# Kernel tuning notes

Hardware: AMD Instinct MI355X
Metric: run time of the kernel (lower is better)

The kernel has to match this reference:

```python
import jax, jax.numpy as jnp
import numpy as np

B, G, K, N, M, E, L = 8, 512, 64, 1024, 128, 4, 5

def _lin(x, w, b):
    return x @ w.T + b

def setup_inputs():
    key = jax.random.key(0)
    ks = jax.random.split(key, 20)
    def nrm(k, shape, s=1.0):
        return jax.random.normal(k, shape, dtype=jnp.float32) * s
    def lin_p(k, out_d, in_d):
        k1, k2 = jax.random.split(k)
        s = 1.0 / float(np.sqrt(in_d))
        return nrm(k1, (out_d, in_d), s), nrm(k2, (out_d,), s)
    inp = {}
    inp["z"] = nrm(ks[0], (B, G, K, M), 0.5)
    inp["hs_grid"] = nrm(ks[1], (B, G, M))
    inp["hs_key"] = nrm(ks[2], (B, K, M))
    inp["lig_rep"] = nrm(ks[3], (B, E))
    inp["hs_rec"] = nrm(ks[4], (B, N, M))
    inp["w_Rl"] = jnp.ones((1,), dtype=jnp.float32)
    inp["w_mask"] = jax.random.randint(ks[5], (B, K), 0, 2)
    dims = {"wra": (M, M), "wrh": (M, M), "wla": (M, M), "wlh": (M, M),
            "z1": (1, M), "wcR": (M, M), "wcl": (M, M), "kR": (M, M),
            "mapL": (L, 2 * M + E), "fin": (1, L)}
    for i, nm in enumerate(dims):
        w, b = lin_p(ks[6 + i], *dims[nm])
        inp[nm + "_w"] = w
        inp[nm + "_b"] = b
    return inp

def reference(z, hs_grid, hs_key, lig_rep, hs_rec, w_Rl, w_mask,
              wra_w, wra_b, wrh_w, wrh_b, wla_w, wla_b, wlh_w, wlh_b,
              z1_w, z1_b, wcR_w, wcR_b, wcl_w, wcl_b, kR_w, kR_b,
              mapL_w, mapL_b, fin_w, fin_b):
    exp_z = jnp.exp(z)                                    # [B,G,K,M]
    zr = exp_z / exp_z.sum(axis=-2, keepdims=True)        # pseudo-softmax over K
    ra = jnp.einsum('bgkm,bkm->bgm', zr, hs_key)          # [B,G,M]
    zl = exp_z / exp_z.sum(axis=-3, keepdims=True)        # pseudo-softmax over G
    la = jnp.einsum('bgkm,bgm->bkm', zl, hs_grid)         # [B,K,M]
    ra_rh = _lin(ra, wra_w, wra_b) + _lin(hs_grid, wrh_w, wrh_b)  # [B,G,M]
    la_lh = _lin(la, wla_w, wla_b) + _lin(hs_key, wlh_w, wlh_b)   # [B,K,M]
    att = _lin(z, z1_w, z1_b)[..., 0]                     # [B,G,K]
    att_l = jax.nn.softmax(att, axis=2).sum(axis=1)       # [B,K]
    att_r = jax.nn.softmax(att, axis=1).sum(axis=2)       # [B,G]
    key_rep = jnp.einsum('bk,bkm->bm', att_l, la_lh)      # [B,M]
    grid_rep = jnp.einsum('bg,bgm->bm', att_r, ra_rh)     # [B,M]
    Rh = _lin(hs_rec, wcR_w, wcR_b)                       # [B,N,M]
    lh = _lin(hs_key, wcl_w, wcl_b)                       # [B,K,M]
    z_Rl = jnp.einsum('bnh,bkh->bnk', Rh, lh)             # [B,N,K]
    masked = jnp.where(w_mask[:, None, :] == 0, jnp.float32(-1e10), w_Rl * z_Rl)
    z_Rl = jax.nn.softmax(masked, axis=1)                 # softmax over N
    kfr = jnp.einsum('bnk,bnh->bkh', z_Rl, hs_rec)        # [B,K,M]
    kfr = _lin(kfr, kR_w, kR_b)
    kfr = jnp.einsum('bk,bkh->bh', att_l, kfr)            # [B,M]
    key_rep = key_rep + kfr
    pair_rep = jnp.concatenate([key_rep, lig_rep, grid_rep], axis=1)  # [B,2M+E]
    pair_rep = _lin(pair_rep, mapL_w, mapL_b)             # [B,L]
    return _lin(pair_rep, fin_w, fin_b)[..., 0]           # [B]
```

## Files before the change

kernel.cpp:

```cpp
#include <hip/hip_runtime.h>

#define Bb 8
#define Gg 512
#define Kk 64
#define Nn 1024
#define Mm 128
#define KM (Kk * Mm)
#define GPB 16
#define NCH 32

struct P7 { const float* p[7]; };

__global__ __launch_bounds__(1024) void kA(
    const float* __restrict__ z, const float* __restrict__ hs_grid,
    const float* __restrict__ hs_key, const float* __restrict__ z1w,
    P7 ptrs, float* __restrict__ wT,
    float* __restrict__ raOut, float* __restrict__ attOut,
    float* __restrict__ laNum, float* __restrict__ laDen)
{
  __shared__ __align__(16) float smem[10240];
  const int bid = blockIdx.x;
  const int t = threadIdx.x;

  if (bid >= Bb * NCH) {
    float* tile = smem;
    const int r = bid - Bb * NCH;
    const int mat = r >> 4, tl = r & 15;
    const int xo = (tl & 3) * 32, y0 = (tl >> 2) * 32;
    const int tx = t & 31, ty = t >> 5;
    const float* src = ptrs.p[mat];
    float* dst = wT + (size_t)mat * Mm * Mm;
    tile[ty * 33 + tx] = src[(size_t)(y0 + ty) * Mm + xo + tx];
    __syncthreads();
    dst[(size_t)(xo + ty) * Mm + y0 + tx] = tile[tx * 33 + ty];
    return;
  }

  float* s_hsgrid = smem;
  float* s_rn     = smem + 2048;
  float* s_rd     = smem + 6144;

  const int b = bid >> 5;
  const int gblk = bid & 31;
  const int lane_m = t & 31;
  const int m4 = lane_m << 2;
  const int kgrp = t >> 5;
  const int wv = t >> 6;

  const float* hgb = hs_grid + ((size_t)b * Gg + gblk * GPB) * Mm;
  for (int idx = t; idx < GPB * Mm; idx += 1024) s_hsgrid[idx] = hgb[idx];

  const int ofs0 = (kgrp * 2) * Mm + m4;
  const int ofs1 = ofs0 + Mm;
  const float4 hk0 = *reinterpret_cast<const float4*>(hs_key + (size_t)b * KM + ofs0);
  const float4 hk1 = *reinterpret_cast<const float4*>(hs_key + (size_t)b * KM + ofs1);

  const float zw0 = z1w[m4], zw1 = z1w[m4 + 1], zw2 = z1w[m4 + 2], zw3 = z1w[m4 + 3];

  float la_n[2][4], la_d[2][4];
#pragma unroll
  for (int i = 0; i < 2; ++i)
#pragma unroll
    for (int j = 0; j < 4; ++j) { la_n[i][j] = 0.f; la_d[i][j] = 0.f; }

  const float* zb = z + ((size_t)b * Gg + gblk * GPB) * (size_t)KM;
  float4 c0 = *reinterpret_cast<const float4*>(zb + ofs0);
  float4 c1 = *reinterpret_cast<const float4*>(zb + ofs1);

  __syncthreads();

  for (int gl = 0; gl < GPB; ++gl) {
    float4 n0 = c0, n1 = c1;
    if (gl < GPB - 1) {
      n0 = *reinterpret_cast<const float4*>(zb + (size_t)(gl + 1) * KM + ofs0);
      n1 = *reinterpret_cast<const float4*>(zb + (size_t)(gl + 1) * KM + ofs1);
    }
    const int g = gblk * GPB + gl;
    const float4 hg = *reinterpret_cast<const float4*>(s_hsgrid + gl * Mm + m4);
    float rn0 = 0, rn1 = 0, rn2 = 0, rn3 = 0, rd0 = 0, rd1 = 0, rd2 = 0, rd3 = 0;
#pragma unroll
    for (int i = 0; i < 2; ++i) {
      const float4 v = (i == 0) ? c0 : c1;
      const float4 hk = (i == 0) ? hk0 : hk1;
      const int k = kgrp * 2 + i;
      const float e0 = __expf(v.x), e1 = __expf(v.y), e2 = __expf(v.z), e3 = __expf(v.w);
      la_n[i][0] += e0 * hg.x; la_n[i][1] += e1 * hg.y; la_n[i][2] += e2 * hg.z; la_n[i][3] += e3 * hg.w;
      la_d[i][0] += e0;        la_d[i][1] += e1;        la_d[i][2] += e2;        la_d[i][3] += e3;
      rn0 += e0 * hk.x; rn1 += e1 * hk.y; rn2 += e2 * hk.z; rn3 += e3 * hk.w;
      rd0 += e0; rd1 += e1; rd2 += e2; rd3 += e3;
      float ap = v.x * zw0 + v.y * zw1 + v.z * zw2 + v.w * zw3;
      ap += __shfl_xor(ap, 16); ap += __shfl_xor(ap, 8); ap += __shfl_xor(ap, 4);
      ap += __shfl_xor(ap, 2);  ap += __shfl_xor(ap, 1);
      if (lane_m == 0) attOut[((size_t)b * Gg + g) * Kk + k] = ap;
    }
    rn0 += __shfl_xor(rn0, 32); rn1 += __shfl_xor(rn1, 32); rn2 += __shfl_xor(rn2, 32); rn3 += __shfl_xor(rn3, 32);
    rd0 += __shfl_xor(rd0, 32); rd1 += __shfl_xor(rd1, 32); rd2 += __shfl_xor(rd2, 32); rd3 += __shfl_xor(rd3, 32);
    float* rnB = s_rn + (gl & 1) * 2048;
    float* rdB = s_rd + (gl & 1) * 2048;
    if ((t & 63) < 32) {
      *reinterpret_cast<float4*>(rnB + wv * Mm + m4) = make_float4(rn0, rn1, rn2, rn3);
      *reinterpret_cast<float4*>(rdB + wv * Mm + m4) = make_float4(rd0, rd1, rd2, rd3);
    }
    __syncthreads();
    if (t < Mm) {
      float num = 0.f, den = 0.f;
#pragma unroll
      for (int ww = 0; ww < 16; ++ww) { num += rnB[ww * Mm + t]; den += rdB[ww * Mm + t]; }
      raOut[((size_t)b * Gg + g) * Mm + t] = num / den;
    }
    c0 = n0; c1 = n1;
  }

  const size_t base = ((size_t)(b * NCH + gblk)) * KM;
#pragma unroll
  for (int i = 0; i < 2; ++i) {
    const int k = kgrp * 2 + i;
    *reinterpret_cast<float4*>(laNum + base + k * Mm + m4) =
        make_float4(la_n[i][0], la_n[i][1], la_n[i][2], la_n[i][3]);
    *reinterpret_cast<float4*>(laDen + base + k * Mm + m4) =
        make_float4(la_d[i][0], la_d[i][1], la_d[i][2], la_d[i][3]);
  }
}

__global__ __launch_bounds__(256) void kB(
    const float* __restrict__ laNum, const float* __restrict__ laDen, float* __restrict__ la,
    const float* __restrict__ att, float* __restrict__ attlP,
    float* __restrict__ attrPM, float* __restrict__ attrPS,
    const float* __restrict__ hs_key, const float* __restrict__ wT,
    const float* __restrict__ wcR_w, const float* __restrict__ wcl_b,
    float* __restrict__ Lk)
{
  __shared__ __align__(16) float smem[1088];
  const int bid = blockIdx.x;
  const int t = threadIdx.x;

  if (bid < 256) {
    const int idx = bid * 256 + t;
    const int b = idx >> 13, r = idx & 8191;
    const float* np = laNum + (size_t)b * NCH * KM + r;
    const float* dp = laDen + (size_t)b * NCH * KM + r;
    float num = 0.f, den = 0.f;
#pragma unroll 8
    for (int p = 0; p < NCH; ++p) { num += np[(size_t)p * KM]; den += dp[(size_t)p * KM]; }
    la[idx] = num / den;
  } else if (bid < 320) {
    const int blk = bid - 256;
    const int b = blk >> 3, p = blk & 7;
    const int w = t >> 6, lane = t & 63;
    float acc = 0.f;
    for (int j = 0; j < 16; ++j) {
      const int g = p * 64 + w * 16 + j;
      const float a = att[((size_t)b * Gg + g) * Kk + lane];
      float mx = a;
      for (int off = 32; off; off >>= 1) mx = fmaxf(mx, __shfl_xor(mx, off));
      const float e = __expf(a - mx);
      float s = e;
      for (int off = 32; off; off >>= 1) s += __shfl_xor(s, off);
      acc += e / s;
    }
    float* sred = smem;
    sred[w * 64 + lane] = acc;
    __syncthreads();
    if (t < 64) attlP[(b * 8 + p) * 64 + t] = sred[t] + sred[64 + t] + sred[128 + t] + sred[192 + t];
  } else if (bid < 384) {
    const int blk = bid - 320;
    const int b = blk >> 3, gc = blk & 7;
    const int k = t & 63, j4 = t >> 6;
    float m = -1e30f, s = 0.f;
    for (int j = 0; j < 16; ++j) {
      const int g = gc * 64 + j4 * 16 + j;
      const float a = att[((size_t)b * Gg + g) * Kk + k];
      if (a > m) { s = s * __expf(m - a) + 1.0f; m = a; }
      else s += __expf(a - m);
    }
    float* sm = smem;
    float* ss = smem + 256;
    sm[j4 * 64 + k] = m; ss[j4 * 64 + k] = s;
    __syncthreads();
    if (t < 64) {
      float M = sm[t];
      for (int q = 1; q < 4; ++q) M = fmaxf(M, sm[q * 64 + t]);
      float S = 0.f;
      for (int q = 0; q < 4; ++q) S += ss[q * 64 + t] * __expf(sm[q * 64 + t] - M);
      attrPM[(b * 8 + gc) * 64 + t] = M;
      attrPS[(b * 8 + gc) * 64 + t] = S;
    }
  } else {
    const int blk = bid - 384;
    const int b = blk >> 3, k8 = blk & 7;
    float* s_lh = smem;
    const int m = t & 127;
    const int half = __builtin_amdgcn_readfirstlane(t >> 7);
    const float* wclT = wT + 5 * 16384;
    {
      const float* keyb = hs_key + ((size_t)b * Kk + k8 * 8 + half * 4) * Mm;
      float a0 = 0.f, a1 = 0.f, a2 = 0.f, a3 = 0.f;
      for (int h4 = 0; h4 < 32; ++h4) {
        const float4 r0v = *reinterpret_cast<const float4*>(keyb + h4 * 4);
        const float4 r1v = *reinterpret_cast<const float4*>(keyb + 128 + h4 * 4);
        const float4 r2v = *reinterpret_cast<const float4*>(keyb + 256 + h4 * 4);
        const float4 r3v = *reinterpret_cast<const float4*>(keyb + 384 + h4 * 4);
        const float w0 = wclT[(size_t)(h4 * 4 + 0) * Mm + m];
        const float w1 = wclT[(size_t)(h4 * 4 + 1) * Mm + m];
        const float w2 = wclT[(size_t)(h4 * 4 + 2) * Mm + m];
        const float w3 = wclT[(size_t)(h4 * 4 + 3) * Mm + m];
        a0 += r0v.x * w0 + r0v.y * w1 + r0v.z * w2 + r0v.w * w3;
        a1 += r1v.x * w0 + r1v.y * w1 + r1v.z * w2 + r1v.w * w3;
        a2 += r2v.x * w0 + r2v.y * w1 + r2v.z * w2 + r2v.w * w3;
        a3 += r3v.x * w0 + r3v.y * w1 + r3v.z * w2 + r3v.w * w3;
      }
      const float bm = wcl_b[m];
      s_lh[(half * 4 + 0) * 132 + m] = a0 + bm;
      s_lh[(half * 4 + 1) * 132 + m] = a1 + bm;
      s_lh[(half * 4 + 2) * 132 + m] = a2 + bm;
      s_lh[(half * 4 + 3) * 132 + m] = a3 + bm;
    }
    __syncthreads();
    {
      const int h = m;
      const int r0 = half * 4;
      float b0 = 0.f, b1 = 0.f, b2 = 0.f, b3 = 0.f;
      for (int mq = 0; mq < 32; ++mq) {
        const float4 L0 = *reinterpret_cast<const float4*>(&s_lh[(r0 + 0) * 132 + mq * 4]);
        const float4 L1 = *reinterpret_cast<const float4*>(&s_lh[(r0 + 1) * 132 + mq * 4]);
        const float4 L2 = *reinterpret_cast<const float4*>(&s_lh[(r0 + 2) * 132 + mq * 4]);
        const float4 L3 = *reinterpret_cast<const float4*>(&s_lh[(r0 + 3) * 132 + mq * 4]);
        const float w0 = wcR_w[(size_t)(mq * 4 + 0) * Mm + h];
        const float w1 = wcR_w[(size_t)(mq * 4 + 1) * Mm + h];
        const float w2 = wcR_w[(size_t)(mq * 4 + 2) * Mm + h];
        const float w3 = wcR_w[(size_t)(mq * 4 + 3) * Mm + h];
        b0 += L0.x * w0 + L0.y * w1 + L0.z * w2 + L0.w * w3;
        b1 += L1.x * w0 + L1.y * w1 + L1.z * w2 + L1.w * w3;
        b2 += L2.x * w0 + L2.y * w1 + L2.z * w2 + L2.w * w3;
        b3 += L3.x * w0 + L3.y * w1 + L3.z * w2 + L3.w * w3;
      }
      const size_t ob = ((size_t)b * Kk + k8 * 8 + r0) * Mm + h;
      Lk[ob] = b0; Lk[ob + Mm] = b1; Lk[ob + 2 * Mm] = b2; Lk[ob + 3 * Mm] = b3;
    }
  }
}

__global__ __launch_bounds__(256) void kC(
    const float* __restrict__ att, const float* __restrict__ attrPM, const float* __restrict__ attrPS,
    float* __restrict__ att_r,
    const float* __restrict__ hs_rec, const float* __restrict__ Lk,
    const int* __restrict__ mask, const float* __restrict__ wRl,
    float* __restrict__ scores, float* __restrict__ pmT, float* __restrict__ psT)
{
  __shared__ __align__(16) float smem[4608];
  const int bid = blockIdx.x;
  const int t = threadIdx.x;

  if (bid < 64) {
    const int b = bid >> 3, gc = bid & 7;
    const int k = t & 63, grp = t >> 6;
    float* Mx = smem;
    float* S = smem + 64;
    if (t < 64) {
      float M = -1e30f;
      for (int p = 0; p < 8; ++p) M = fmaxf(M, attrPM[(b * 8 + p) * 64 + t]);
      float s = 0.f;
      for (int p = 0; p < 8; ++p) s += attrPS[(b * 8 + p) * 64 + t] * __expf(attrPM[(b * 8 + p) * 64 + t] - M);
      Mx[t] = M; S[t] = s;
    }
    __syncthreads();
    const float Mk = Mx[k], Sk = S[k];
    for (int j = 0; j < 16; ++j) {
      const int g = gc * 64 + grp * 16 + j;
      float p = __expf(att[((size_t)b * Gg + g) * Kk + k] - Mk) / Sk;
      for (int off = 32; off; off >>= 1) p += __shfl_xor(p, off);
      if (k == 0) att_r[b * Gg + g] = p;
    }
  } else {
    const int vb = bid - 64;
    const int b = vb >> 6, ntile = vb & 63;
    const int n0 = ntile * 16;
    const int k = t & 63;
    const int hq = __builtin_amdgcn_readfirstlane(t >> 6);
    float rLk[32];
    {
      const float* Lp = Lk + ((size_t)b * Kk + k) * Mm + hq * 32;
#pragma unroll
      for (int j = 0; j < 8; ++j) {
        const float4 v = *reinterpret_cast<const float4*>(Lp + j * 4);
        rLk[j * 4 + 0] = v.x; rLk[j * 4 + 1] = v.y;
        rLk[j * 4 + 2] = v.z; rLk[j * 4 + 3] = v.w;
      }
    }
    float acc[16];
    const float* rb = hs_rec + ((size_t)b * Nn + n0) * Mm + hq * 32;
#pragma unroll
    for (int r = 0; r < 16; ++r) {
      const float* rp = rb + r * Mm;
      float s = 0.f;
#pragma unroll
      for (int j4 = 0; j4 < 8; ++j4) {
        const float4 rv = *reinterpret_cast<const float4*>(rp + j4 * 4);
        s += rv.x * rLk[j4 * 4] + rv.y * rLk[j4 * 4 + 1] +
             rv.z * rLk[j4 * 4 + 2] + rv.w * rLk[j4 * 4 + 3];
      }
      acc[r] = s;
    }
    float* s_acc = smem;
    float* s_m   = smem + 4096;
    float* s_s   = smem + 4352;
#pragma unroll
    for (int r = 0; r < 16; ++r) s_acc[(hq * 16 + r) * 64 + k] = acc[r];
    __syncthreads();
    const float wv = wRl[0];
    const bool msk = (mask[b * Kk + k] == 0);
    float m = -3.0e38f, ssum = 0.f;
    for (int q = 0; q < 4; ++q) {
      const int idx = q * 256 + t;
      const int r = idx >> 6, kk = idx & 63;
      float v = s_acc[r * 64 + kk] + s_acc[(16 + r) * 64 + kk] +
                s_acc[(32 + r) * 64 + kk] + s_acc[(48 + r) * 64 + kk];
      v = msk ? -1e10f : wv * v;
      scores[((size_t)b * Nn + n0 + r) * Kk + kk] = v;
      if (v > m) { ssum = ssum * __expf(m - v) + 1.0f; m = v; }
      else ssum += __expf(v - m);
    }
    s_m[hq * 64 + k] = m; s_s[hq * 64 + k] = ssum;
    __syncthreads();
    if (t < 64) {
      float M = fmaxf(fmaxf(s_m[t], s_m[64 + t]), fmaxf(s_m[128 + t], s_m[192 + t]));
      float S = 0.f;
#pragma unroll
      for (int q = 0; q < 4; ++q) S += s_s[q * 64 + t] * __expf(s_m[q * 64 + t] - M);
      pmT[((size_t)b * 64 + ntile) * 64 + t] = M;
      psT[((size_t)b * 64 + ntile) * 64 + t] = S;
    }
  }
}

__global__ __launch_bounds__(512) void kD(
    const float* __restrict__ scores, const float* __restrict__ hs_rec,
    const float* __restrict__ pmT, const float* __restrict__ psT,
    const float* __restrict__ attlP, const float* __restrict__ att_r,
    const float* __restrict__ ra, const float* __restrict__ hs_grid,
    const float* __restrict__ la, const float* __restrict__ hs_key,
    float* __restrict__ uP, float* __restrict__ w1P, float* __restrict__ w2P,
    float* __restrict__ w0P, float* __restrict__ v1, float* __restrict__ v2,
    float* __restrict__ sAv)
{
  __shared__ float sm[1280];
  __shared__ float s_attl[64];
  __shared__ float sM[64], sSi[64];
  const int bid = blockIdx.x;
  const int t = threadIdx.x;

  if (bid < 64) {
    const int b = bid >> 3, nc = bid & 7;
    if (t < 64) {
      float a = 0.f;
      for (int p = 0; p < 8; ++p) a += attlP[(b * 8 + p) * 64 + t];
      s_attl[t] = a;
      float M = -3.0e38f;
      for (int nt = 0; nt < 64; ++nt) M = fmaxf(M, pmT[((size_t)b * 64 + nt) * 64 + t]);
      float S = 0.f;
      for (int nt = 0; nt < 64; ++nt)
        S += psT[((size_t)b * 64 + nt) * 64 + t] * __expf(pmT[((size_t)b * 64 + nt) * 64 + t] - M);
      sM[t] = M; sSi[t] = 1.0f / S;
    }
    __syncthreads();
    const int n = t >> 2, ks = t & 3;
    const float* sc = scores + ((size_t)b * Nn + nc * 128 + n) * Kk + ks * 16;
    float qp = 0.f;
#pragma unroll
    for (int j = 0; j < 16; ++j) {
      const int k = ks * 16 + j;
      qp += s_attl[k] * __expf(sc[j] - sM[k]) * sSi[k];
    }
    sm[n * 4 + ks] = qp;
    __syncthreads();
    float* q = sm + 512;
    if (t < 128) q[t] = sm[t * 4] + sm[t * 4 + 1] + sm[t * 4 + 2] + sm[t * 4 + 3];
    __syncthreads();
    const int h = t & 127, nq = t >> 7;
    float acc = 0.f;
    const float* hr = hs_rec + ((size_t)b * Nn + nc * 128 + nq * 32) * Mm + h;
    for (int j = 0; j < 32; ++j) acc += q[nq * 32 + j] * hr[(size_t)j * Mm];
    float* red = sm + 640;
    red[nq * 128 + h] = acc;
    __syncthreads();
    if (t < 128) uP[((size_t)b * 8 + nc) * 128 + t] = red[t] + red[128 + t] + red[256 + t] + red[384 + t];
  } else if (bid < 128) {
    const int blk = bid - 64;
    const int b = blk >> 3, gc = blk & 7;
    float* s_ar = sm + 1152;
    if (t < 64) s_ar[t] = att_r[b * Gg + gc * 64 + t];
    __syncthreads();
    const int h = t & 127, gq = t >> 7;
    float a1 = 0.f, a2 = 0.f;
    const float* rp = ra + ((size_t)b * Gg + gc * 64 + gq * 16) * Mm + h;
    const float* gp = hs_grid + ((size_t)b * Gg + gc * 64 + gq * 16) * Mm + h;
    for (int j = 0; j < 16; ++j) {
      const float w = s_ar[gq * 16 + j];
      a1 += w * rp[(size_t)j * Mm];
      a2 += w * gp[(size_t)j * Mm];
    }
    float* r1 = sm;
    float* r2 = sm + 512;
    r1[gq * 128 + h] = a1; r2[gq * 128 + h] = a2;
    __syncthreads();
    if (t < 128) {
      w1P[((size_t)b * 8 + gc) * 128 + t] = r1[t] + r1[128 + t] + r1[256 + t] + r1[384 + t];
      w2P[((size_t)b * 8 + gc) * 128 + t] = r2[t] + r2[128 + t] + r2[256 + t] + r2[384 + t];
    }
    if (t == 0) {
      float s = 0.f;
      for (int j = 0; j < 64; ++j) s += s_ar[j];
      w0P[b * 8 + gc] = s;
    }
  } else {
    const int b = bid - 128;
    if (t < 64) {
      float a = 0.f;
      for (int p = 0; p < 8; ++p) a += attlP[(b * 8 + p) * 64 + t];
      s_attl[t] = a;
    }
    __syncthreads();
    const int h = t & 127, kq = t >> 7;
    float a1 = 0.f, a2 = 0.f;
    const float* lp = la + ((size_t)b * Kk + kq * 16) * Mm + h;
    const float* kp = hs_key + ((size_t)b * Kk + kq * 16) * Mm + h;
    for (int j = 0; j < 16; ++j) {
      const float w = s_attl[kq * 16 + j];
      a1 += w * lp[(size_t)j * Mm];
      a2 += w * kp[(size_t)j * Mm];
    }
    float* r1 = sm;
    float* r2 = sm + 512;
    r1[kq * 128 + h] = a1; r2[kq * 128 + h] = a2;
    __syncthreads();
    if (t < 128) {
      v1[b * 128 + t] = r1[t] + r1[128 + t] + r1[256 + t] + r1[384 + t];
      v2[b * 128 + t] = r2[t] + r2[128 + t] + r2[256 + t] + r2[384 + t];
    }
    if (t == 0) {
      float s = 0.f;
      for (int j = 0; j < 64; ++j) s += s_attl[j];
      sAv[b] = s;
    }
  }
}

__global__ __launch_bounds__(1024) void kE(
    const float* __restrict__ uP, const float* __restrict__ w1P, const float* __restrict__ w2P,
    const float* __restrict__ w0P, const float* __restrict__ v1, const float* __restrict__ v2,
    const float* __restrict__ sAv, const float* __restrict__ wT,
    const float* __restrict__ wra_b, const float* __restrict__ wrh_b,
    const float* __restrict__ wla_b, const float* __restrict__ wlh_b,
    const float* __restrict__ kR_b, const float* __restrict__ lig_rep,
    const float* __restrict__ mapL_w, const float* __restrict__ mapL_b,
    const float* __restrict__ fin_w, const float* __restrict__ fin_b,
    float* __restrict__ out)
{
  __shared__ float sV1[128], sV2[128], sU[128], sW1[128], sW2[128];
  __shared__ float sPair[264];
  __shared__ float sRed[2][8][128];
  __shared__ float s5[8];
  __shared__ float sSc[2];
  const int b = blockIdx.x, t = threadIdx.x;
  const int m = t & 127, hf = t >> 7;

  if (t < 128) {
    float u = 0.f, w1 = 0.f, w2 = 0.f;
    for (int c = 0; c < 8; ++c) {
      u  += uP[((size_t)b * 8 + c) * 128 + t];
      w1 += w1P[((size_t)b * 8 + c) * 128 + t];
      w2 += w2P[((size_t)b * 8 + c) * 128 + t];
    }
    sU[t] = u; sW1[t] = w1; sW2[t] = w2;
    sV1[t] = v1[b * 128 + t]; sV2[t] = v2[b * 128 + t];
  }
  if (t == 0) {
    float s = 0.f;
    for (int c = 0; c < 8; ++c) s += w0P[b * 8 + c];
    sSc[0] = s;
    sSc[1] = sAv[b];
  }
  __syncthreads();

  const float* wraT = wT;
  const float* wrhT = wT + 1 * 16384;
  const float* wlaT = wT + 2 * 16384;
  const float* wlhT = wT + 3 * 16384;
  const float* kRT  = wT + 6 * 16384;
  float key = 0.f, grd = 0.f;
  for (int h = hf * 16; h < hf * 16 + 16; ++h) {
    key += sV1[h] * wlaT[h * Mm + m] + sV2[h] * wlhT[h * Mm + m] + sU[h] * kRT[h * Mm + m];
    grd += sW1[h] * wraT[h * Mm + m] + sW2[h] * wrhT[h * Mm + m];
  }
  sRed[0][hf][m] = key; sRed[1][hf][m] = grd;
  __syncthreads();
  if (t < 128) {
    const float sR = sSc[0], sA = sSc[1];
    float kk = 0.f, gg = 0.f;
#pragma unroll
    for (int q = 0; q < 8; ++q) { kk += sRed[0][q][t]; gg += sRed[1][q][t]; }
    sPair[t] = kk + sA * (wla_b[t] + wlh_b[t] + kR_b[t]);
    sPair[132 + t] = gg + sR * (wra_b[t] + wrh_b[t]);
  }
  if (t < 4) sPair[128 + t] = lig_rep[b * 4 + t];
  __syncthreads();

  const int wq = t >> 6, lane = t & 63;
  if (wq < 5) {
    float acc = 0.f;
    for (int c = lane; c < 260; c += 64) acc += sPair[c] * mapL_w[wq * 260 + c];
    for (int off = 32; off; off >>= 1) acc += __shfl_xor(acc, off);
    if (lane == 0) s5[wq] = acc + mapL_b[wq];
  }
  __syncthreads();
  if (t == 0) {
    float o = fin_b[0];
    for (int l = 0; l < 5; ++l) o += s5[l] * fin_w[l];
    out[b] = o;
  }
}

extern "C" void kernel_launch(void* const* d_in, const int* in_sizes, int n_in,
                              void* d_out, int out_size, void* d_ws, size_t ws_size,
                              hipStream_t stream) {
  const float* z       = (const float*)d_in[0];
  const float* hs_grid = (const float*)d_in[1];
  const float* hs_key  = (const float*)d_in[2];
  const float* lig_rep = (const float*)d_in[3];
  const float* hs_rec  = (const float*)d_in[4];
  const float* w_Rl    = (const float*)d_in[5];
  const int*   w_mask  = (const int*)d_in[6];
  const float* wra_w = (const float*)d_in[7];  const float* wra_b = (const float*)d_in[8];
  const float* wrh_w = (const float*)d_in[9];  const float* wrh_b = (const float*)d_in[10];
  const float* wla_w = (const float*)d_in[11]; const float* wla_b = (const float*)d_in[12];
  const float* wlh_w = (const float*)d_in[13]; const float* wlh_b = (const float*)d_in[14];
  const float* z1_w  = (const float*)d_in[15];
  const float* wcR_w = (const float*)d_in[17]; const float* wcR_b = (const float*)d_in[18];
  const float* wcl_w = (const float*)d_in[19]; const float* wcl_b = (const float*)d_in[20];
  const float* kR_w  = (const float*)d_in[21]; const float* kR_b  = (const float*)d_in[22];
  const float* mapL_w = (const float*)d_in[23]; const float* mapL_b = (const float*)d_in[24];
  const float* fin_w  = (const float*)d_in[25]; const float* fin_b  = (const float*)d_in[26];
  float* out = (float*)d_out;

  float* w = (float*)d_ws;
  float* wT    = w;
  float* ra    = wT + 7 * 16384;
  float* att   = ra + Bb * Gg * Mm;
  float* laNum = att + Bb * Gg * Kk;
  float* laDen = laNum + Bb * NCH * Kk * Mm;
  float* la    = laDen + Bb * NCH * Kk * Mm;
  float* attlP = la + Bb * Kk * Mm;
  float* attrPM = attlP + Bb * 8 * 64;
  float* attrPS = attrPM + Bb * 8 * 64;
  float* att_r = attrPS + Bb * 8 * 64;
  float* Lk    = att_r + Bb * Gg;
  float* scores = Lk + Bb * Kk * Mm;

  float* pmT  = laNum;
  float* psT  = laNum + 32768;
  float* uP   = laNum + 65536;
  float* w1P  = laNum + 73728;
  float* w2P  = laNum + 81920;
  float* w0P  = laNum + 90112;
  float* v1   = laNum + 90176;
  float* v2   = laNum + 91200;
  float* sAv  = laNum + 92224;

  P7 ptrs;
  ptrs.p[0] = wra_w; ptrs.p[1] = wrh_w; ptrs.p[2] = wla_w; ptrs.p[3] = wlh_w;
  ptrs.p[4] = wcR_w; ptrs.p[5] = wcl_w; ptrs.p[6] = kR_w;

  kA<<<Bb * NCH + 112, 1024, 0, stream>>>(z, hs_grid, hs_key, z1_w, ptrs, wT,
                                          ra, att, laNum, laDen);
  kB<<<448, 256, 0, stream>>>(laNum, laDen, la, att, attlP, attrPM, attrPS,
                              hs_key, wT, wcR_w, wcl_b, Lk);
  kC<<<576, 256, 0, stream>>>(att, attrPM, attrPS, att_r, hs_rec, Lk,
                              w_mask, w_Rl, scores, pmT, psT);
  kD<<<136, 512, 0, stream>>>(scores, hs_rec, pmT, psT, attlP, att_r,
                              ra, hs_grid, la, hs_key,
                              uP, w1P, w2P, w0P, v1, v2, sAv);
  kE<<<Bb, 1024, 0, stream>>>(uP, w1P, w2P, w0P, v1, v2, sAv, wT,
                              wra_b, wrh_b, wla_b, wlh_b, kR_b, lig_rep,
                              mapL_w, mapL_b, fin_w, fin_b, out);
}
```

Measured before the change: 89.06 us.

## Fold final linear layers into projected weight vectors and merge pipeline into three kernels

```diff
diff --git a/kernel.cpp b/kernel.cpp
--- a/kernel.cpp
+++ b/kernel.cpp
@@ -9,151 +9,239 @@
 #define GPB 16
 #define NCH 32
 
-struct P7 { const float* p[7]; };
-
-__global__ __launch_bounds__(1024) void kA(
-    const float* __restrict__ z, const float* __restrict__ hs_grid,
-    const float* __restrict__ hs_key, const float* __restrict__ z1w,
-    P7 ptrs, float* __restrict__ wT,
-    float* __restrict__ raOut, float* __restrict__ attOut,
-    float* __restrict__ laNum, float* __restrict__ laDen)
-{
-  __shared__ __align__(16) float smem[10240];
+struct K1Args {
+  const float *z, *hs_grid, *hs_key, *z1w;
+  const float *wra_w, *wrh_w, *wla_w, *wlh_w, *kR_w;
+  const float *wla_b, *wlh_b, *kR_b, *wra_b, *wrh_b;
+  const float *wcl_w, *wcl_b, *wcR_w;
+  const float *mapL_w, *mapL_b, *fin_w, *fin_b;
+  float *att, *laNum, *laDen, *rdot, *Lk, *gbuf;
+};
+
+__global__ __launch_bounds__(1024) void K1(K1Args a) {
+  __shared__ __align__(16) float smem[10496];
   const int bid = blockIdx.x;
   const int t = threadIdx.x;
 
-  if (bid >= Bb * NCH) {
-    float* tile = smem;
-    const int r = bid - Bb * NCH;
-    const int mat = r >> 4, tl = r & 15;
-    const int xo = (tl & 3) * 32, y0 = (tl >> 2) * 32;
-    const int tx = t & 31, ty = t >> 5;
-    const float* src = ptrs.p[mat];
-    float* dst = wT + (size_t)mat * Mm * Mm;
-    tile[ty * 33 + tx] = src[(size_t)(y0 + ty) * Mm + xo + tx];
-    __syncthreads();
-    dst[(size_t)(xo + ty) * Mm + y0 + tx] = tile[tx * 33 + ty];
-    return;
-  }
-
-  float* s_hsgrid = smem;
-  float* s_rn     = smem + 2048;
-  float* s_rd     = smem + 6144;
-
-  const int b = bid >> 5;
-  const int gblk = bid & 31;
-  const int lane_m = t & 31;
-  const int m4 = lane_m << 2;
-  const int kgrp = t >> 5;
-  const int wv = t >> 6;
-
-  const float* hgb = hs_grid + ((size_t)b * Gg + gblk * GPB) * Mm;
-  for (int idx = t; idx < GPB * Mm; idx += 1024) s_hsgrid[idx] = hgb[idx];
-
-  const int ofs0 = (kgrp * 2) * Mm + m4;
-  const int ofs1 = ofs0 + Mm;
-  const float4 hk0 = *reinterpret_cast<const float4*>(hs_key + (size_t)b * KM + ofs0);
-  const float4 hk1 = *reinterpret_cast<const float4*>(hs_key + (size_t)b * KM + ofs1);
-
-  const float zw0 = z1w[m4], zw1 = z1w[m4 + 1], zw2 = z1w[m4 + 2], zw3 = z1w[m4 + 3];
-
-  float la_n[2][4], la_d[2][4];
-#pragma unroll
-  for (int i = 0; i < 2; ++i)
-#pragma unroll
-    for (int j = 0; j < 4; ++j) { la_n[i][j] = 0.f; la_d[i][j] = 0.f; }
-
-  const float* zb = z + ((size_t)b * Gg + gblk * GPB) * (size_t)KM;
-  float4 c0 = *reinterpret_cast<const float4*>(zb + ofs0);
-  float4 c1 = *reinterpret_cast<const float4*>(zb + ofs1);
-
-  __syncthreads();
-
-  for (int gl = 0; gl < GPB; ++gl) {
-    float4 n0 = c0, n1 = c1;
-    if (gl < GPB - 1) {
-      n0 = *reinterpret_cast<const float4*>(zb + (size_t)(gl + 1) * KM + ofs0);
-      n1 = *reinterpret_cast<const float4*>(zb + (size_t)(gl + 1) * KM + ofs1);
-    }
-    const int g = gblk * GPB + gl;
-    const float4 hg = *reinterpret_cast<const float4*>(s_hsgrid + gl * Mm + m4);
-    float rn0 = 0, rn1 = 0, rn2 = 0, rn3 = 0, rd0 = 0, rd1 = 0, rd2 = 0, rd3 = 0;
+  if (bid < 256) {
+    float* s_gw     = smem;
+    float* s_hsgrid = smem + 256;
+    float* s_rn     = smem + 2304;
+    float* s_rd     = smem + 6400;
+    float* s_fvecG  = smem + 2304;
+
+    const int b = bid >> 5;
+    const int gblk = bid & 31;
+    const int lane_m = t & 31;
+    const int m4 = lane_m << 2;
+    const int kgrp = t >> 5;
+    const int wv = t >> 6;
+
+    const int ofs0 = (kgrp * 2) * Mm + m4;
+    const int ofs1 = ofs0 + Mm;
+    const float* zb = a.z + ((size_t)b * Gg + gblk * GPB) * (size_t)KM;
+    float4 c0 = *reinterpret_cast<const float4*>(zb + ofs0);
+    float4 c1 = *reinterpret_cast<const float4*>(zb + ofs1);
+
+    const float* hgb = a.hs_grid + ((size_t)b * Gg + gblk * GPB) * Mm;
+    for (int idx = t; idx < GPB * Mm; idx += 1024) s_hsgrid[idx] = hgb[idx];
+
+    const float4 hk0 = *reinterpret_cast<const float4*>(a.hs_key + (size_t)b * KM + ofs0);
+    const float4 hk1 = *reinterpret_cast<const float4*>(a.hs_key + (size_t)b * KM + ofs1);
+    const float zw0 = a.z1w[m4], zw1 = a.z1w[m4 + 1], zw2 = a.z1w[m4 + 2], zw3 = a.z1w[m4 + 3];
+
+    if (t < 128) {
+      float f = 0.f;
+#pragma unroll
+      for (int l = 0; l < 5; ++l) f += a.fin_w[l] * a.mapL_w[l * 260 + 132 + t];
+      s_fvecG[t] = f;
+    }
+    __syncthreads();
+    if (t < 256) {
+      const int h = t & 127;
+      const float* W = (t >> 7) ? a.wrh_w : a.wra_w;
+      float g = 0.f;
+      for (int mm = 0; mm < 128; ++mm) g += s_fvecG[mm] * W[(size_t)mm * Mm + h];
+      s_gw[t] = g;
+    }
+    __syncthreads();
+
+    float la_n[2][4], la_d[2][4];
+#pragma unroll
+    for (int i = 0; i < 2; ++i)
+#pragma unroll
+      for (int j = 0; j < 4; ++j) { la_n[i][j] = 0.f; la_d[i][j] = 0.f; }
+
+    for (int gl = 0; gl < GPB; ++gl) {
+      float4 n0 = c0, n1 = c1;
+      if (gl < GPB - 1) {
+        n0 = *reinterpret_cast<const float4*>(zb + (size_t)(gl + 1) * KM + ofs0);
+        n1 = *reinterpret_cast<const float4*>(zb + (size_t)(gl + 1) * KM + ofs1);
+      }
+      const int g = gblk * GPB + gl;
+      const float4 hg = *reinterpret_cast<const float4*>(s_hsgrid + gl * Mm + m4);
+      float rn0 = 0, rn1 = 0, rn2 = 0, rn3 = 0, rd0 = 0, rd1 = 0, rd2 = 0, rd3 = 0;
+#pragma unroll
+      for (int i = 0; i < 2; ++i) {
+        const float4 v = (i == 0) ? c0 : c1;
+        const float4 hk = (i == 0) ? hk0 : hk1;
+        const int k = kgrp * 2 + i;
+        const float e0 = __expf(v.x), e1 = __expf(v.y), e2 = __expf(v.z), e3 = __expf(v.w);
+        la_n[i][0] += e0 * hg.x; la_n[i][1] += e1 * hg.y; la_n[i][2] += e2 * hg.z; la_n[i][3] += e3 * hg.w;
+        la_d[i][0] += e0;        la_d[i][1] += e1;        la_d[i][2] += e2;        la_d[i][3] += e3;
+        rn0 += e0 * hk.x; rn1 += e1 * hk.y; rn2 += e2 * hk.z; rn3 += e3 * hk.w;
+        rd0 += e0; rd1 += e1; rd2 += e2; rd3 += e3;
+        float ap = v.x * zw0 + v.y * zw1 + v.z * zw2 + v.w * zw3;
+        ap += __shfl_xor(ap, 16); ap += __shfl_xor(ap, 8); ap += __shfl_xor(ap, 4);
+        ap += __shfl_xor(ap, 2);  ap += __shfl_xor(ap, 1);
+        if (lane_m == 0) a.att[((size_t)b * Gg + g) * Kk + k] = ap;
+      }
+      rn0 += __shfl_xor(rn0, 32); rn1 += __shfl_xor(rn1, 32); rn2 += __shfl_xor(rn2, 32); rn3 += __shfl_xor(rn3, 32);
+      rd0 += __shfl_xor(rd0, 32); rd1 += __shfl_xor(rd1, 32); rd2 += __shfl_xor(rd2, 32); rd3 += __shfl_xor(rd3, 32);
+      float* rnB = s_rn + (gl & 1) * 2048;
+      float* rdB = s_rd + (gl & 1) * 2048;
+      if ((t & 63) < 32) {
+        *reinterpret_cast<float4*>(rnB + wv * Mm + m4) = make_float4(rn0, rn1, rn2, rn3);
+        *reinterpret_cast<float4*>(rdB + wv * Mm + m4) = make_float4(rd0, rd1, rd2, rd3);
+      }
+      __syncthreads();
+      if (t < 64) {
+        float num0 = 0, den0 = 0, num1 = 0, den1 = 0;
+#pragma unroll
+        for (int ww = 0; ww < 16; ++ww) {
+          num0 += rnB[ww * Mm + t];      den0 += rdB[ww * Mm + t];
+          num1 += rnB[ww * Mm + t + 64]; den1 += rdB[ww * Mm + t + 64];
+        }
+        float val = s_gw[t] * (num0 / den0) + s_gw[t + 64] * (num1 / den1)
+                  + s_gw[128 + t] * s_hsgrid[gl * Mm + t]
+                  + s_gw[192 + t] * s_hsgrid[gl * Mm + t + 64];
+        val += __shfl_xor(val, 32); val += __shfl_xor(val, 16); val += __shfl_xor(val, 8);
+        val += __shfl_xor(val, 4);  val += __shfl_xor(val, 2);  val += __shfl_xor(val, 1);
+        if (t == 0) a.rdot[(size_t)b * Gg + g] = val;
+      }
+      c0 = n0; c1 = n1;
+    }
+
+    const size_t base = ((size_t)(b * NCH + gblk)) * KM;
 #pragma unroll
     for (int i = 0; i < 2; ++i) {
-      const float4 v = (i == 0) ? c0 : c1;
-      const float4 hk = (i == 0) ? hk0 : hk1;
       const int k = kgrp * 2 + i;
-      const float e0 = __expf(v.x), e1 = __expf(v.y), e2 = __expf(v.z), e3 = __expf(v.w);
-      la_n[i][0] += e0 * hg.x; la_n[i][1] += e1 * hg.y; la_n[i][2] += e2 * hg.z; la_n[i][3] += e3 * hg.w;
-      la_d[i][0] += e0;        la_d[i][1] += e1;        la_d[i][2] += e2;        la_d[i][3] += e3;
-      rn0 += e0 * hk.x; rn1 += e1 * hk.y; rn2 += e2 * hk.z; rn3 += e3 * hk.w;
-      rd0 += e0; rd1 += e1; rd2 += e2; rd3 += e3;
-      float ap = v.x * zw0 + v.y * zw1 + v.z * zw2 + v.w * zw3;
-      ap += __shfl_xor(ap, 16); ap += __shfl_xor(ap, 8); ap += __shfl_xor(ap, 4);
-      ap += __shfl_xor(ap, 2);  ap += __shfl_xor(ap, 1);
-      if (lane_m == 0) attOut[((size_t)b * Gg + g) * Kk + k] = ap;
-    }
-    rn0 += __shfl_xor(rn0, 32); rn1 += __shfl_xor(rn1, 32); rn2 += __shfl_xor(rn2, 32); rn3 += __shfl_xor(rn3, 32);
-    rd0 += __shfl_xor(rd0, 32); rd1 += __shfl_xor(rd1, 32); rd2 += __shfl_xor(rd2, 32); rd3 += __shfl_xor(rd3, 32);
-    float* rnB = s_rn + (gl & 1) * 2048;
-    float* rdB = s_rd + (gl & 1) * 2048;
-    if ((t & 63) < 32) {
-      *reinterpret_cast<float4*>(rnB + wv * Mm + m4) = make_float4(rn0, rn1, rn2, rn3);
-      *reinterpret_cast<float4*>(rdB + wv * Mm + m4) = make_float4(rd0, rd1, rd2, rd3);
-    }
-    __syncthreads();
-    if (t < Mm) {
-      float num = 0.f, den = 0.f;
-#pragma unroll
-      for (int ww = 0; ww < 16; ++ww) { num += rnB[ww * Mm + t]; den += rdB[ww * Mm + t]; }
-      raOut[((size_t)b * Gg + g) * Mm + t] = num / den;
-    }
-    c0 = n0; c1 = n1;
-  }
-
-  const size_t base = ((size_t)(b * NCH + gblk)) * KM;
-#pragma unroll
-  for (int i = 0; i < 2; ++i) {
-    const int k = kgrp * 2 + i;
-    *reinterpret_cast<float4*>(laNum + base + k * Mm + m4) =
-        make_float4(la_n[i][0], la_n[i][1], la_n[i][2], la_n[i][3]);
-    *reinterpret_cast<float4*>(laDen + base + k * Mm + m4) =
-        make_float4(la_d[i][0], la_d[i][1], la_d[i][2], la_d[i][3]);
+      *reinterpret_cast<float4*>(a.laNum + base + k * Mm + m4) =
+          make_float4(la_n[i][0], la_n[i][1], la_n[i][2], la_n[i][3]);
+      *reinterpret_cast<float4*>(a.laDen + base + k * Mm + m4) =
+          make_float4(la_d[i][0], la_d[i][1], la_d[i][2], la_d[i][3]);
+    }
+  } else if (bid < 320) {
+    float* s_w  = smem;
+    float* s_lh = smem + 4224;
+    const int blk = bid - 256;
+    const int b = blk >> 3, k8 = blk & 7;
+    const int m = t & 127, kq = t >> 7;
+    const int k = k8 * 8 + kq;
+    float lh = 0.f;
+    for (int hc = 0; hc < 4; ++hc) {
+      for (int i = t; i < 4096; i += 1024) {
+        const int mm = i >> 5, hh = i & 31;
+        s_w[hh * 132 + mm] = a.wcl_w[(size_t)mm * Mm + hc * 32 + hh];
+      }
+      __syncthreads();
+      const float* keyb = a.hs_key + ((size_t)b * Kk + k) * Mm + hc * 32;
+      for (int hh = 0; hh < 32; ++hh) lh += keyb[hh] * s_w[hh * 132 + m];
+      __syncthreads();
+    }
+    s_lh[kq * 132 + m] = lh + a.wcl_b[m];
+    __syncthreads();
+    float acc = 0.f;
+    for (int mm = 0; mm < 128; ++mm)
+      acc += s_lh[kq * 132 + mm] * a.wcR_w[(size_t)mm * Mm + m];
+    a.Lk[((size_t)b * Kk + k) * Mm + m] = acc;
+  } else {
+    float* s_fvec = smem;
+    float* s_red  = smem + 260;
+    if (t < 260) {
+      float f = 0.f;
+#pragma unroll
+      for (int l = 0; l < 5; ++l) f += a.fin_w[l] * a.mapL_w[l * 260 + t];
+      s_fvec[t] = f;
+    }
+    __syncthreads();
+    const int h = t & 127, sel = t >> 7;
+    if (sel < 3) {
+      const float* W = (sel == 0) ? a.wla_w : (sel == 1) ? a.wlh_w : a.kR_w;
+      float g = 0.f;
+      for (int mm = 0; mm < 128; ++mm) g += s_fvec[mm] * W[(size_t)mm * Mm + h];
+      a.gbuf[sel * 128 + h] = g;
+    }
+    if (t < 128) {
+      s_red[t] = s_fvec[t] * (a.wla_b[t] + a.wlh_b[t] + a.kR_b[t]);
+      s_red[128 + t] = s_fvec[132 + t] * (a.wra_b[t] + a.wrh_b[t]);
+    }
+    __syncthreads();
+    if (t == 0) {
+      float c1 = 0.f, c2 = 0.f;
+      for (int i = 0; i < 128; ++i) { c1 += s_red[i]; c2 += s_red[128 + i]; }
+      float C = a.fin_b[0];
+#pragma unroll
+      for (int l = 0; l < 5; ++l) C += a.fin_w[l] * a.mapL_b[l];
+      a.gbuf[384] = c1; a.gbuf[385] = c2; a.gbuf[386] = C;
+#pragma unroll
+      for (int e = 0; e < 4; ++e) a.gbuf[387 + e] = s_fvec[128 + e];
+    }
   }
 }
 
-__global__ __launch_bounds__(256) void kB(
-    const float* __restrict__ laNum, const float* __restrict__ laDen, float* __restrict__ la,
-    const float* __restrict__ att, float* __restrict__ attlP,
-    float* __restrict__ attrPM, float* __restrict__ attrPS,
-    const float* __restrict__ hs_key, const float* __restrict__ wT,
-    const float* __restrict__ wcR_w, const float* __restrict__ wcl_b,
-    float* __restrict__ Lk)
-{
-  __shared__ __align__(16) float smem[1088];
+struct K2Args {
+  const float *laNum, *laDen, *hs_key, *att, *rdot, *Lk, *hs_rec;
+  const int *mask;
+  const float *wRl, *gbuf;
+  float *attlP, *gridpart, *sRv, *pmT, *psT, *PSpT, *laDot, *keyDot;
+};
+
+__global__ __launch_bounds__(256) void K2(K2Args a) {
+  __shared__ __align__(16) float smem[4944];
   const int bid = blockIdx.x;
   const int t = threadIdx.x;
 
-  if (bid < 256) {
-    const int idx = bid * 256 + t;
-    const int b = idx >> 13, r = idx & 8191;
-    const float* np = laNum + (size_t)b * NCH * KM + r;
-    const float* dp = laDen + (size_t)b * NCH * KM + r;
-    float num = 0.f, den = 0.f;
+  if (bid < 64) {
+    const int b = bid >> 3, k8 = bid & 7;
+    const int m = t & 127, kh = t >> 7;
+    const float g1 = a.gbuf[m], g2 = a.gbuf[128 + m];
+    float* sl = smem;
+    float* sk = smem + 1056;
+#pragma unroll
+    for (int i = 0; i < 4; ++i) {
+      const int k = k8 * 8 + kh * 4 + i;
+      const float* np = a.laNum + (size_t)b * NCH * KM + (size_t)k * Mm + m;
+      const float* dp = a.laDen + (size_t)b * NCH * KM + (size_t)k * Mm + m;
+      float num = 0.f, den = 0.f;
 #pragma unroll 8
-    for (int p = 0; p < NCH; ++p) { num += np[(size_t)p * KM]; den += dp[(size_t)p * KM]; }
-    la[idx] = num / den;
-  } else if (bid < 320) {
-    const int blk = bid - 256;
+      for (int p = 0; p < NCH; ++p) { num += np[(size_t)p * KM]; den += dp[(size_t)p * KM]; }
+      sl[(kh * 4 + i) * 132 + m] = g1 * (num / den);
+      sk[(kh * 4 + i) * 132 + m] = g2 * a.hs_key[((size_t)b * Kk + k) * Mm + m];
+    }
+    __syncthreads();
+    const int rid = t >> 5, l32 = t & 31;
+    float s1 = sl[rid * 132 + l32] + sl[rid * 132 + l32 + 32] +
+               sl[rid * 132 + l32 + 64] + sl[rid * 132 + l32 + 96];
+    float s2 = sk[rid * 132 + l32] + sk[rid * 132 + l32 + 32] +
+               sk[rid * 132 + l32 + 64] + sk[rid * 132 + l32 + 96];
+#pragma unroll
+    for (int off = 16; off; off >>= 1) { s1 += __shfl_xor(s1, off); s2 += __shfl_xor(s2, off); }
+    if (l32 == 0) {
+      a.laDot[b * Kk + k8 * 8 + rid] = s1;
+      a.keyDot[b * Kk + k8 * 8 + rid] = s2;
+    }
+  } else if (bid < 128) {
+    const int blk = bid - 64;
     const int b = blk >> 3, p = blk & 7;
     const int w = t >> 6, lane = t & 63;
     float acc = 0.f;
     for (int j = 0; j < 16; ++j) {
       const int g = p * 64 + w * 16 + j;
-      const float a = att[((size_t)b * Gg + g) * Kk + lane];
-      float mx = a;
+      const float av = a.att[((size_t)b * Gg + g) * Kk + lane];
+      float mx = av;
       for (int off = 32; off; off >>= 1) mx = fmaxf(mx, __shfl_xor(mx, off));
-      const float e = __expf(a - mx);
+      const float e = __expf(av - mx);
       float s = e;
       for (int off = 32; off; off >>= 1) s += __shfl_xor(s, off);
       acc += e / s;
@@ -161,125 +249,61 @@
     float* sred = smem;
     sred[w * 64 + lane] = acc;
     __syncthreads();
-    if (t < 64) attlP[(b * 8 + p) * 64 + t] = sred[t] + sred[64 + t] + sred[128 + t] + sred[192 + t];
-  } else if (bid < 384) {
-    const int blk = bid - 320;
-    const int b = blk >> 3, gc = blk & 7;
-    const int k = t & 63, j4 = t >> 6;
-    float m = -1e30f, s = 0.f;
-    for (int j = 0; j < 16; ++j) {
-      const int g = gc * 64 + j4 * 16 + j;
-      const float a = att[((size_t)b * Gg + g) * Kk + k];
-      if (a > m) { s = s * __expf(m - a) + 1.0f; m = a; }
-      else s += __expf(a - m);
-    }
-    float* sm = smem;
-    float* ss = smem + 256;
-    sm[j4 * 64 + k] = m; ss[j4 * 64 + k] = s;
+    if (t < 64) a.attlP[(b * 8 + p) * 64 + t] = sred[t] + sred[64 + t] + sred[128 + t] + sred[192 + t];
+  } else if (bid < 136) {
+    const int b = bid - 128;
+    float* sM_ = smem;
+    float* sS_ = smem + 64;
+    float* spm = smem + 128;
+    float* sps = smem + 384;
+    const int k = t & 63, gq = t >> 6;
+    const float* ab = a.att + (size_t)b * Gg * Kk;
+    float m_ = -3.0e38f, s_ = 0.f;
+    for (int j = 0; j < 128; ++j) {
+      const float av = ab[(size_t)(gq * 128 + j) * Kk + k];
+      if (av > m_) { s_ = s_ * __expf(m_ - av) + 1.0f; m_ = av; }
+      else s_ += __expf(av - m_);
+    }
+    spm[gq * 64 + k] = m_; sps[gq * 64 + k] = s_;
     __syncthreads();
     if (t < 64) {
-      float M = sm[t];
-      for (int q = 1; q < 4; ++q) M = fmaxf(M, sm[q * 64 + t]);
+      float M = spm[t];
+      for (int q = 1; q < 4; ++q) M = fmaxf(M, spm[q * 64 + t]);
       float S = 0.f;
-      for (int q = 0; q < 4; ++q) S += ss[q * 64 + t] * __expf(sm[q * 64 + t] - M);
-      attrPM[(b * 8 + gc) * 64 + t] = M;
-      attrPS[(b * 8 + gc) * 64 + t] = S;
+      for (int q = 0; q < 4; ++q) S += sps[q * 64 + t] * __expf(spm[q * 64 + t] - M);
+      sM_[t] = M; sS_[t] = S;
+    }
+    __syncthreads();
+    const float Mk = sM_[k], Sk = sS_[k];
+    float accG = 0.f, accS = 0.f;
+    for (int j = 0; j < 128; ++j) {
+      const int g = gq * 128 + j;
+      float e = __expf(ab[(size_t)g * Kk + k] - Mk) / Sk;
+      for (int off = 32; off; off >>= 1) e += __shfl_xor(e, off);
+      if (k == 0) { accG += e * a.rdot[(size_t)b * Gg + g]; accS += e; }
+    }
+    __syncthreads();
+    if (k == 0) { spm[gq] = accG; sps[gq] = accS; }
+    __syncthreads();
+    if (t == 0) {
+      a.gridpart[b] = spm[0] + spm[1] + spm[2] + spm[3];
+      a.sRv[b] = sps[0] + sps[1] + sps[2] + sps[3];
     }
   } else {
-    const int blk = bid - 384;
-    const int b = blk >> 3, k8 = blk & 7;
-    float* s_lh = smem;
-    const int m = t & 127;
-    const int half = __builtin_amdgcn_readfirstlane(t >> 7);
-    const float* wclT = wT + 5 * 16384;
-    {
-      const float* keyb = hs_key + ((size_t)b * Kk + k8 * 8 + half * 4) * Mm;
-      float a0 = 0.f, a1 = 0.f, a2 = 0.f, a3 = 0.f;
-      for (int h4 = 0; h4 < 32; ++h4) {
-        const float4 r0v = *reinterpret_cast<const float4*>(keyb + h4 * 4);
-        const float4 r1v = *reinterpret_cast<const float4*>(keyb + 128 + h4 * 4);
-        const float4 r2v = *reinterpret_cast<const float4*>(keyb + 256 + h4 * 4);
-        const float4 r3v = *reinterpret_cast<const float4*>(keyb + 384 + h4 * 4);
-        const float w0 = wclT[(size_t)(h4 * 4 + 0) * Mm + m];
-        const float w1 = wclT[(size_t)(h4 * 4 + 1) * Mm + m];
-        const float w2 = wclT[(size_t)(h4 * 4 + 2) * Mm + m];
-        const float w3 = wclT[(size_t)(h4 * 4 + 3) * Mm + m];
-        a0 += r0v.x * w0 + r0v.y * w1 + r0v.z * w2 + r0v.w * w3;
-        a1 += r1v.x * w0 + r1v.y * w1 + r1v.z * w2 + r1v.w * w3;
-        a2 += r2v.x * w0 + r2v.y * w1 + r2v.z * w2 + r2v.w * w3;
-        a3 += r3v.x * w0 + r3v.y * w1 + r3v.z * w2 + r3v.w * w3;
-      }
-      const float bm = wcl_b[m];
-      s_lh[(half * 4 + 0) * 132 + m] = a0 + bm;
-      s_lh[(half * 4 + 1) * 132 + m] = a1 + bm;
-      s_lh[(half * 4 + 2) * 132 + m] = a2 + bm;
-      s_lh[(half * 4 + 3) * 132 + m] = a3 + bm;
-    }
-    __syncthreads();
-    {
-      const int h = m;
-      const int r0 = half * 4;
-      float b0 = 0.f, b1 = 0.f, b2 = 0.f, b3 = 0.f;
-      for (int mq = 0; mq < 32; ++mq) {
-        const float4 L0 = *reinterpret_cast<const float4*>(&s_lh[(r0 + 0) * 132 + mq * 4]);
-        const float4 L1 = *reinterpret_cast<const float4*>(&s_lh[(r0 + 1) * 132 + mq * 4]);
-        const float4 L2 = *reinterpret_cast<const float4*>(&s_lh[(r0 + 2) * 132 + mq * 4]);
-        const float4 L3 = *reinterpret_cast<const float4*>(&s_lh[(r0 + 3) * 132 + mq * 4]);
-        const float w0 = wcR_w[(size_t)(mq * 4 + 0) * Mm + h];
-        const float w1 = wcR_w[(size_t)(mq * 4 + 1) * Mm + h];
-        const float w2 = wcR_w[(size_t)(mq * 4 + 2) * Mm + h];
-        const float w3 = wcR_w[(size_t)(mq * 4 + 3) * Mm + h];
-        b0 += L0.x * w0 + L0.y * w1 + L0.z * w2 + L0.w * w3;
-        b1 += L1.x * w0 + L1.y * w1 + L1.z * w2 + L1.w * w3;
-        b2 += L2.x * w0 + L2.y * w1 + L2.z * w2 + L2.w * w3;
-        b3 += L3.x * w0 + L3.y * w1 + L3.z * w2 + L3.w * w3;
-      }
-      const size_t ob = ((size_t)b * Kk + k8 * 8 + r0) * Mm + h;
-      Lk[ob] = b0; Lk[ob + Mm] = b1; Lk[ob + 2 * Mm] = b2; Lk[ob + 3 * Mm] = b3;
-    }
-  }
-}
-
-__global__ __launch_bounds__(256) void kC(
-    const float* __restrict__ att, const float* __restrict__ attrPM, const float* __restrict__ attrPS,
-    float* __restrict__ att_r,
-    const float* __restrict__ hs_rec, const float* __restrict__ Lk,
-    const int* __restrict__ mask, const float* __restrict__ wRl,
-    float* __restrict__ scores, float* __restrict__ pmT, float* __restrict__ psT)
-{
-  __shared__ __align__(16) float smem[4608];
-  const int bid = blockIdx.x;
-  const int t = threadIdx.x;
-
-  if (bid < 64) {
-    const int b = bid >> 3, gc = bid & 7;
-    const int k = t & 63, grp = t >> 6;
-    float* Mx = smem;
-    float* S = smem + 64;
-    if (t < 64) {
-      float M = -1e30f;
-      for (int p = 0; p < 8; ++p) M = fmaxf(M, attrPM[(b * 8 + p) * 64 + t]);
-      float s = 0.f;
-      for (int p = 0; p < 8; ++p) s += attrPS[(b * 8 + p) * 64 + t] * __expf(attrPM[(b * 8 + p) * 64 + t] - M);
-      Mx[t] = M; S[t] = s;
-    }
-    __syncthreads();
-    const float Mk = Mx[k], Sk = S[k];
-    for (int j = 0; j < 16; ++j) {
-      const int g = gc * 64 + grp * 16 + j;
-      float p = __expf(att[((size_t)b * Gg + g) * Kk + k] - Mk) / Sk;
-      for (int off = 32; off; off >>= 1) p += __shfl_xor(p, off);
-      if (k == 0) att_r[b * Gg + g] = p;
-    }
-  } else {
-    const int vb = bid - 64;
+    const int vb = bid - 136;
     const int b = vb >> 6, ntile = vb & 63;
     const int n0 = ntile * 16;
     const int k = t & 63;
     const int hq = __builtin_amdgcn_readfirstlane(t >> 6);
+    float* s_acc = smem;
+    float* s_m   = smem + 4096;
+    float* s_s   = smem + 4352;
+    float* s_p   = smem + 4608;
+    float* s_ru4 = smem + 4864;
+    float* s_ru  = smem + 4928;
     float rLk[32];
     {
-      const float* Lp = Lk + ((size_t)b * Kk + k) * Mm + hq * 32;
+      const float* Lp = a.Lk + ((size_t)b * Kk + k) * Mm + hq * 32;
 #pragma unroll
       for (int j = 0; j < 8; ++j) {
         const float4 v = *reinterpret_cast<const float4*>(Lp + j * 4);
@@ -288,7 +312,7 @@
       }
     }
     float acc[16];
-    const float* rb = hs_rec + ((size_t)b * Nn + n0) * Mm + hq * 32;
+    const float* rb = a.hs_rec + ((size_t)b * Nn + n0) * Mm + hq * 32;
 #pragma unroll
     for (int r = 0; r < 16; ++r) {
       const float* rp = rb + r * Mm;
@@ -301,221 +325,88 @@
       }
       acc[r] = s;
     }
-    float* s_acc = smem;
-    float* s_m   = smem + 4096;
-    float* s_s   = smem + 4352;
 #pragma unroll
     for (int r = 0; r < 16; ++r) s_acc[(hq * 16 + r) * 64 + k] = acc[r];
-    __syncthreads();
-    const float wv = wRl[0];
-    const bool msk = (mask[b * Kk + k] == 0);
-    float m = -3.0e38f, ssum = 0.f;
+    if (t < 64) {
+      const int rt = t >> 2, hc = t & 3;
+      const float* rp = a.hs_rec + ((size_t)b * Nn + n0 + rt) * Mm + hc * 32;
+      const float* gu = a.gbuf + 256 + hc * 32;
+      float s = 0.f;
+#pragma unroll
+      for (int j = 0; j < 32; ++j) s += gu[j] * rp[j];
+      s_ru4[rt * 4 + hc] = s;
+    }
+    __syncthreads();
+    if (t < 16) s_ru[t] = s_ru4[t * 4] + s_ru4[t * 4 + 1] + s_ru4[t * 4 + 2] + s_ru4[t * 4 + 3];
+    __syncthreads();
+    const float wv = a.wRl[0];
+    const bool msk = (a.mask[b * Kk + k] == 0);
+    float m = -3.0e38f, ssum = 0.f, psum = 0.f;
+#pragma unroll
     for (int q = 0; q < 4; ++q) {
       const int idx = q * 256 + t;
-      const int r = idx >> 6, kk = idx & 63;
-      float v = s_acc[r * 64 + kk] + s_acc[(16 + r) * 64 + kk] +
-                s_acc[(32 + r) * 64 + kk] + s_acc[(48 + r) * 64 + kk];
+      const int r = idx >> 6;
+      float v = s_acc[(r & 15) * 64 + k] + s_acc[(16 + (r & 15)) * 64 + k] +
+                s_acc[(32 + (r & 15)) * 64 + k] + s_acc[(48 + (r & 15)) * 64 + k];
       v = msk ? -1e10f : wv * v;
-      scores[((size_t)b * Nn + n0 + r) * Kk + kk] = v;
-      if (v > m) { ssum = ssum * __expf(m - v) + 1.0f; m = v; }
-      else ssum += __expf(v - m);
-    }
-    s_m[hq * 64 + k] = m; s_s[hq * 64 + k] = ssum;
+      const float runow = s_ru[r & 15];
+      if (v > m) {
+        const float sc = __expf(m - v);
+        ssum = ssum * sc + 1.0f; psum = psum * sc + runow; m = v;
+      } else {
+        const float e = __expf(v - m);
+        ssum += e; psum += e * runow;
+      }
+    }
+    s_m[hq * 64 + k] = m; s_s[hq * 64 + k] = ssum; s_p[hq * 64 + k] = psum;
     __syncthreads();
     if (t < 64) {
       float M = fmaxf(fmaxf(s_m[t], s_m[64 + t]), fmaxf(s_m[128 + t], s_m[192 + t]));
-      float S = 0.f;
-#pragma unroll
-      for (int q = 0; q < 4; ++q) S += s_s[q * 64 + t] * __expf(s_m[q * 64 + t] - M);
-      pmT[((size_t)b * 64 + ntile) * 64 + t] = M;
-      psT[((size_t)b * 64 + ntile) * 64 + t] = S;
+      float S = 0.f, P = 0.f;
+#pragma unroll
+      for (int q = 0; q < 4; ++q) {
+        const float e = __expf(s_m[q * 64 + t] - M);
+        S += s_s[q * 64 + t] * e; P += s_p[q * 64 + t] * e;
+      }
+      const size_t o = ((size_t)b * 64 + ntile) * 64 + t;
+      a.pmT[o] = M; a.psT[o] = S; a.PSpT[o] = P;
     }
   }
 }
 
-__global__ __launch_bounds__(512) void kD(
-    const float* __restrict__ scores, const float* __restrict__ hs_rec,
-    const float* __restrict__ pmT, const float* __restrict__ psT,
-    const float* __restrict__ attlP, const float* __restrict__ att_r,
-    const float* __restrict__ ra, const float* __restrict__ hs_grid,
-    const float* __restrict__ la, const float* __restrict__ hs_key,
-    float* __restrict__ uP, float* __restrict__ w1P, float* __restrict__ w2P,
-    float* __restrict__ w0P, float* __restrict__ v1, float* __restrict__ v2,
-    float* __restrict__ sAv)
-{
-  __shared__ float sm[1280];
-  __shared__ float s_attl[64];
-  __shared__ float sM[64], sSi[64];
-  const int bid = blockIdx.x;
-  const int t = threadIdx.x;
-
-  if (bid < 64) {
-    const int b = bid >> 3, nc = bid & 7;
-    if (t < 64) {
-      float a = 0.f;
-      for (int p = 0; p < 8; ++p) a += attlP[(b * 8 + p) * 64 + t];
-      s_attl[t] = a;
-      float M = -3.0e38f;
-      for (int nt = 0; nt < 64; ++nt) M = fmaxf(M, pmT[((size_t)b * 64 + nt) * 64 + t]);
-      float S = 0.f;
-      for (int nt = 0; nt < 64; ++nt)
-        S += psT[((size_t)b * 64 + nt) * 64 + t] * __expf(pmT[((size_t)b * 64 + nt) * 64 + t] - M);
-      sM[t] = M; sSi[t] = 1.0f / S;
-    }
-    __syncthreads();
-    const int n = t >> 2, ks = t & 3;
-    const float* sc = scores + ((size_t)b * Nn + nc * 128 + n) * Kk + ks * 16;
-    float qp = 0.f;
-#pragma unroll
-    for (int j = 0; j < 16; ++j) {
-      const int k = ks * 16 + j;
-      qp += s_attl[k] * __expf(sc[j] - sM[k]) * sSi[k];
-    }
-    sm[n * 4 + ks] = qp;
-    __syncthreads();
-    float* q = sm + 512;
-    if (t < 128) q[t] = sm[t * 4] + sm[t * 4 + 1] + sm[t * 4 + 2] + sm[t * 4 + 3];
-    __syncthreads();
-    const int h = t & 127, nq = t >> 7;
-    float acc = 0.f;
-    const float* hr = hs_rec + ((size_t)b * Nn + nc * 128 + nq * 32) * Mm + h;
-    for (int j = 0; j < 32; ++j) acc += q[nq * 32 + j] * hr[(size_t)j * Mm];
-    float* red = sm + 640;
-    red[nq * 128 + h] = acc;
-    __syncthreads();
-    if (t < 128) uP[((size_t)b * 8 + nc) * 128 + t] = red[t] + red[128 + t] + red[256 + t] + red[384 + t];
-  } else if (bid < 128) {
-    const int blk = bid - 64;
-    const int b = blk >> 3, gc = blk & 7;
-    float* s_ar = sm + 1152;
-    if (t < 64) s_ar[t] = att_r[b * Gg + gc * 64 + t];
-    __syncthreads();
-    const int h = t & 127, gq = t >> 7;
-    float a1 = 0.f, a2 = 0.f;
-    const float* rp = ra + ((size_t)b * Gg + gc * 64 + gq * 16) * Mm + h;
-    const float* gp = hs_grid + ((size_t)b * Gg + gc * 64 + gq * 16) * Mm + h;
-    for (int j = 0; j < 16; ++j) {
-      const float w = s_ar[gq * 16 + j];
-      a1 += w * rp[(size_t)j * Mm];
-      a2 += w * gp[(size_t)j * Mm];
-    }
-    float* r1 = sm;
-    float* r2 = sm + 512;
-    r1[gq * 128 + h] = a1; r2[gq * 128 + h] = a2;
-    __syncthreads();
-    if (t < 128) {
-      w1P[((size_t)b * 8 + gc) * 128 + t] = r1[t] + r1[128 + t] + r1[256 + t] + r1[384 + t];
-      w2P[((size_t)b * 8 + gc) * 128 + t] = r2[t] + r2[128 + t] + r2[256 + t] + r2[384 + t];
-    }
-    if (t == 0) {
-      float s = 0.f;
-      for (int j = 0; j < 64; ++j) s += s_ar[j];
-      w0P[b * 8 + gc] = s;
-    }
-  } else {
-    const int b = bid - 128;
-    if (t < 64) {
-      float a = 0.f;
-      for (int p = 0; p < 8; ++p) a += attlP[(b * 8 + p) * 64 + t];
-      s_attl[t] = a;
-    }
-    __syncthreads();
-    const int h = t & 127, kq = t >> 7;
-    float a1 = 0.f, a2 = 0.f;
-    const float* lp = la + ((size_t)b * Kk + kq * 16) * Mm + h;
-    const float* kp = hs_key + ((size_t)b * Kk + kq * 16) * Mm + h;
-    for (int j = 0; j < 16; ++j) {
-      const float w = s_attl[kq * 16 + j];
-      a1 += w * lp[(size_t)j * Mm];
-      a2 += w * kp[(size_t)j * Mm];
-    }
-    float* r1 = sm;
-    float* r2 = sm + 512;
-    r1[kq * 128 + h] = a1; r2[kq * 128 + h] = a2;
-    __syncthreads();
-    if (t < 128) {
-      v1[b * 128 + t] = r1[t] + r1[128 + t] + r1[256 + t] + r1[384 + t];
-      v2[b * 128 + t] = r2[t] + r2[128 + t] + r2[256 + t] + r2[384 + t];
-    }
-    if (t == 0) {
-      float s = 0.f;
-      for (int j = 0; j < 64; ++j) s += s_attl[j];
-      sAv[b] = s;
-    }
-  }
-}
-
-__global__ __launch_bounds__(1024) void kE(
-    const float* __restrict__ uP, const float* __restrict__ w1P, const float* __restrict__ w2P,
-    const float* __restrict__ w0P, const float* __restrict__ v1, const float* __restrict__ v2,
-    const float* __restrict__ sAv, const float* __restrict__ wT,
-    const float* __restrict__ wra_b, const float* __restrict__ wrh_b,
-    const float* __restrict__ wla_b, const float* __restrict__ wlh_b,
-    const float* __restrict__ kR_b, const float* __restrict__ lig_rep,
-    const float* __restrict__ mapL_w, const float* __restrict__ mapL_b,
-    const float* __restrict__ fin_w, const float* __restrict__ fin_b,
+__global__ __launch_bounds__(64) void K3(
+    const float* __restrict__ attlP, const float* __restrict__ pmT,
+    const float* __restrict__ psT, const float* __restrict__ PSpT,
+    const float* __restrict__ laDot, const float* __restrict__ keyDot,
+    const float* __restrict__ gridpart, const float* __restrict__ sRv,
+    const float* __restrict__ gbuf, const float* __restrict__ lig_rep,
     float* __restrict__ out)
 {
-  __shared__ float sV1[128], sV2[128], sU[128], sW1[128], sW2[128];
-  __shared__ float sPair[264];
-  __shared__ float sRed[2][8][128];
-  __shared__ float s5[8];
-  __shared__ float sSc[2];
   const int b = blockIdx.x, t = threadIdx.x;
-  const int m = t & 127, hf = t >> 7;
-
-  if (t < 128) {
-    float u = 0.f, w1 = 0.f, w2 = 0.f;
-    for (int c = 0; c < 8; ++c) {
-      u  += uP[((size_t)b * 8 + c) * 128 + t];
-      w1 += w1P[((size_t)b * 8 + c) * 128 + t];
-      w2 += w2P[((size_t)b * 8 + c) * 128 + t];
-    }
-    sU[t] = u; sW1[t] = w1; sW2[t] = w2;
-    sV1[t] = v1[b * 128 + t]; sV2[t] = v2[b * 128 + t];
+  float attl = 0.f;
+#pragma unroll
+  for (int p = 0; p < 8; ++p) attl += attlP[(b * 8 + p) * 64 + t];
+  float M = -3.0e38f, S = 0.f, P = 0.f;
+  for (int nt = 0; nt < 64; ++nt) {
+    const size_t o = ((size_t)b * 64 + nt) * 64 + t;
+    const float pm_ = pmT[o], ps_ = psT[o], pp = PSpT[o];
+    if (pm_ > M) {
+      const float sc = __expf(M - pm_);
+      S = S * sc + ps_; P = P * sc + pp; M = pm_;
+    } else {
+      const float e = __expf(pm_ - M);
+      S += ps_ * e; P += pp * e;
+    }
   }
+  float val = attl * (laDot[b * 64 + t] + keyDot[b * 64 + t] + P / S);
+  float sa = attl;
+#pragma unroll
+  for (int off = 32; off; off >>= 1) { val += __shfl_xor(val, off); sa += __shfl_xor(sa, off); }
   if (t == 0) {
-    float s = 0.f;
-    for (int c = 0; c < 8; ++c) s += w0P[b * 8 + c];
-    sSc[0] = s;
-    sSc[1] = sAv[b];
-  }
-  __syncthreads();
-
-  const float* wraT = wT;
-  const float* wrhT = wT + 1 * 16384;
-  const float* wlaT = wT + 2 * 16384;
-  const float* wlhT = wT + 3 * 16384;
-  const float* kRT  = wT + 6 * 16384;
-  float key = 0.f, grd = 0.f;
-  for (int h = hf * 16; h < hf * 16 + 16; ++h) {
-    key += sV1[h] * wlaT[h * Mm + m] + sV2[h] * wlhT[h * Mm + m] + sU[h] * kRT[h * Mm + m];
-    grd += sW1[h] * wraT[h * Mm + m] + sW2[h] * wrhT[h * Mm + m];
-  }
-  sRed[0][hf][m] = key; sRed[1][hf][m] = grd;
-  __syncthreads();
-  if (t < 128) {
-    const float sR = sSc[0], sA = sSc[1];
-    float kk = 0.f, gg = 0.f;
-#pragma unroll
-    for (int q = 0; q < 8; ++q) { kk += sRed[0][q][t]; gg += sRed[1][q][t]; }
-    sPair[t] = kk + sA * (wla_b[t] + wlh_b[t] + kR_b[t]);
-    sPair[132 + t] = gg + sR * (wra_b[t] + wrh_b[t]);
-  }
-  if (t < 4) sPair[128 + t] = lig_rep[b * 4 + t];
-  __syncthreads();
-
-  const int wq = t >> 6, lane = t & 63;
-  if (wq < 5) {
-    float acc = 0.f;
-    for (int c = lane; c < 260; c += 64) acc += sPair[c] * mapL_w[wq * 260 + c];
-    for (int off = 32; off; off >>= 1) acc += __shfl_xor(acc, off);
-    if (lane == 0) s5[wq] = acc + mapL_b[wq];
-  }
-  __syncthreads();
-  if (t == 0) {
-    float o = fin_b[0];
-    for (int l = 0; l < 5; ++l) o += s5[l] * fin_w[l];
+    const float c1 = gbuf[384], c2 = gbuf[385], C = gbuf[386];
+    float o = val + gridpart[b] + sa * c1 + sRv[b] * c2 + C;
+#pragma unroll
+    for (int e = 0; e < 4; ++e) o += gbuf[387 + e] * lig_rep[b * 4 + e];
     out[b] = o;
   }
 }
@@ -523,63 +414,54 @@
 extern "C" void kernel_launch(void* const* d_in, const int* in_sizes, int n_in,
                               void* d_out, int out_size, void* d_ws, size_t ws_size,
                               hipStream_t stream) {
-  const float* z       = (const float*)d_in[0];
-  const float* hs_grid = (const float*)d_in[1];
-  const float* hs_key  = (const float*)d_in[2];
-  const float* lig_rep = (const float*)d_in[3];
-  const float* hs_rec  = (const float*)d_in[4];
-  const float* w_Rl    = (const float*)d_in[5];
-  const int*   w_mask  = (const int*)d_in[6];
-  const float* wra_w = (const float*)d_in[7];  const float* wra_b = (const float*)d_in[8];
-  const float* wrh_w = (const float*)d_in[9];  const float* wrh_b = (const float*)d_in[10];
-  const float* wla_w = (const float*)d_in[11]; const float* wla_b = (const float*)d_in[12];
-  const float* wlh_w = (const float*)d_in[13]; const float* wlh_b = (const float*)d_in[14];
-  const float* z1_w  = (const float*)d_in[15];
-  const float* wcR_w = (const float*)d_in[17]; const float* wcR_b = (const float*)d_in[18];
-  const float* wcl_w = (const float*)d_in[19]; const float* wcl_b = (const float*)d_in[20];
-  const float* kR_w  = (const float*)d_in[21]; const float* kR_b  = (const float*)d_in[22];
-  const float* mapL_w = (const float*)d_in[23]; const float* mapL_b = (const float*)d_in[24];
-  const float* fin_w  = (const float*)d_in[25]; const float* fin_b  = (const float*)d_in[26];
-  float* out = (float*)d_out;
-
   float* w = (float*)d_ws;
-  float* wT    = w;
-  float* ra    = wT + 7 * 16384;
-  float* att   = ra + Bb * Gg * Mm;
+  float* gbuf  = w;
+  float* att   = gbuf + 512;
   float* laNum = att + Bb * Gg * Kk;
-  float* laDen = laNum + Bb * NCH * Kk * Mm;
-  float* la    = laDen + Bb * NCH * Kk * Mm;
-  float* attlP = la + Bb * Kk * Mm;
-  float* attrPM = attlP + Bb * 8 * 64;
-  float* attrPS = attrPM + Bb * 8 * 64;
-  float* att_r = attrPS + Bb * 8 * 64;
-  float* Lk    = att_r + Bb * Gg;
-  float* scores = Lk + Bb * Kk * Mm;
-
-  float* pmT  = laNum;
-  float* psT  = laNum + 32768;
-  float* uP   = laNum + 65536;
-  float* w1P  = laNum + 73728;
-  float* w2P  = laNum + 81920;
-  float* w0P  = laNum + 90112;
-  float* v1   = laNum + 90176;
-  float* v2   = laNum + 91200;
-  float* sAv  = laNum + 92224;
-
-  P7 ptrs;
-  ptrs.p[0] = wra_w; ptrs.p[1] = wrh_w; ptrs.p[2] = wla_w; ptrs.p[3] = wlh_w;
-  ptrs.p[4] = wcR_w; ptrs.p[5] = wcl_w; ptrs.p[6] = kR_w;
-
-  kA<<<Bb * NCH + 112, 1024, 0, stream>>>(z, hs_grid, hs_key, z1_w, ptrs, wT,
-                                          ra, att, laNum, laDen);
-  kB<<<448, 256, 0, stream>>>(laNum, laDen, la, att, attlP, attrPM, attrPS,
-                              hs_key, wT, wcR_w, wcl_b, Lk);
-  kC<<<576, 256, 0, stream>>>(att, attrPM, attrPS, att_r, hs_rec, Lk,
-                              w_mask, w_Rl, scores, pmT, psT);
-  kD<<<136, 512, 0, stream>>>(scores, hs_rec, pmT, psT, attlP, att_r,
-                              ra, hs_grid, la, hs_key,
-                              uP, w1P, w2P, w0P, v1, v2, sAv);
-  kE<<<Bb, 1024, 0, stream>>>(uP, w1P, w2P, w0P, v1, v2, sAv, wT,
-                              wra_b, wrh_b, wla_b, wlh_b, kR_b, lig_rep,
-                              mapL_w, mapL_b, fin_w, fin_b, out);
+  float* laDen = laNum + Bb * NCH * KM;
+  float* rdot  = laDen + Bb * NCH * KM;
+  float* Lk    = rdot + Bb * Gg;
+  float* attlP = Lk + Bb * Kk * Mm;
+  float* pmT   = attlP + Bb * 8 * 64;
+  float* psT   = pmT + Bb * 64 * 64;
+  float* PSpT  = psT + Bb * 64 * 64;
+  float* laDot = PSpT + Bb * 64 * 64;
+  float* keyDot = laDot + Bb * Kk;
+  float* gridpart = keyDot + Bb * Kk;
+  float* sRv   = gridpart + Bb;
+
+  K1Args a1;
+  a1.z = (const float*)d_in[0];
+  a1.hs_grid = (const float*)d_in[1];
+  a1.hs_key = (const float*)d_in[2];
+  a1.z1w = (const float*)d_in[15];
+  a1.wra_w = (const float*)d_in[7];  a1.wra_b = (const float*)d_in[8];
+  a1.wrh_w = (const float*)d_in[9];  a1.wrh_b = (const float*)d_in[10];
+  a1.wla_w = (const float*)d_in[11]; a1.wla_b = (const float*)d_in[12];
+  a1.wlh_w = (const float*)d_in[13]; a1.wlh_b = (const float*)d_in[14];
+  a1.wcl_w = (const float*)d_in[19]; a1.wcl_b = (const float*)d_in[20];
+  a1.wcR_w = (const float*)d_in[17];
+  a1.kR_w  = (const float*)d_in[21]; a1.kR_b = (const float*)d_in[22];
+  a1.mapL_w = (const float*)d_in[23]; a1.mapL_b = (const float*)d_in[24];
+  a1.fin_w = (const float*)d_in[25]; a1.fin_b = (const float*)d_in[26];
+  a1.att = att; a1.laNum = laNum; a1.laDen = laDen;
+  a1.rdot = rdot; a1.Lk = Lk; a1.gbuf = gbuf;
+
+  K2Args a2;
+  a2.laNum = laNum; a2.laDen = laDen;
+  a2.hs_key = (const float*)d_in[2];
+  a2.att = att; a2.rdot = rdot; a2.Lk = Lk;
+  a2.hs_rec = (const float*)d_in[4];
+  a2.mask = (const int*)d_in[6];
+  a2.wRl = (const float*)d_in[5];
+  a2.gbuf = gbuf;
+  a2.attlP = attlP; a2.gridpart = gridpart; a2.sRv = sRv;
+  a2.pmT = pmT; a2.psT = psT; a2.PSpT = PSpT;
+  a2.laDot = laDot; a2.keyDot = keyDot;
+
+  K1<<<321, 1024, 0, stream>>>(a1);
+  K2<<<648, 256, 0, stream>>>(a2);
+  K3<<<Bb, 64, 0, stream>>>(attlP, pmT, psT, PSpT, laDot, keyDot,
+                            gridpart, sRv, gbuf, (const float*)d_in[3],
+                            (float*)d_out);
 }
```

Result: slower. 175.0 us (+96.5%).
